# Optimization experiments

Hardware: AMD Instinct MI355X
Metric: run time of the kernel (lower is better)

## Reference

```python
import jax, jax.numpy as jnp
import numpy as np

B, F, L, P, H = 32, 64, 8192, 96, 8
HD = F // H
EPS_ATTN = 1e-6
EPS_REVIN = 1e-5
EPS_LN = 1e-5


def setup_inputs() -> dict:
    key = jax.random.key(0)
    ks = jax.random.split(key, 8)
    f32 = jnp.float32
    return {
        'x': jax.random.normal(ks[0], (B, F, L), dtype=f32),
        'gamma': jnp.ones((1, 1, F), dtype=f32),
        'beta': jnp.zeros((1, 1, F), dtype=f32),
        'ln_w': jnp.ones((F,), dtype=f32),
        'ln_b': jnp.zeros((F,), dtype=f32),
        'Wq': 0.05 * jax.random.normal(ks[1], (F, F), dtype=f32),
        'bq': jnp.zeros((F,), dtype=f32),
        'Wk': 0.05 * jax.random.normal(ks[2], (F, F), dtype=f32),
        'bk': jnp.zeros((F,), dtype=f32),
        'Wv': 0.05 * jax.random.normal(ks[3], (F, F), dtype=f32),
        'bv': jnp.zeros((F,), dtype=f32),
        'Wo': 0.05 * jax.random.normal(ks[4], (F, F), dtype=f32),
        'bo': jnp.zeros((F,), dtype=f32),
        'Wlin': 0.01 * jax.random.normal(ks[5], (P, L), dtype=f32),
        'blin': jnp.zeros((P,), dtype=f32),
        'Wp': 0.1 * jax.random.normal(ks[6], (1, F), dtype=f32),
        'bp': jnp.zeros((1,), dtype=f32),
    }


def _phi(t):
    # feature map: elu(x) + 1 (non-negative)
    return jax.nn.elu(t) + 1.0


def _layernorm(h, w, b):
    mu = jnp.mean(h, axis=-1, keepdims=True)
    var = jnp.mean(jnp.square(h - mu), axis=-1, keepdims=True)
    return (h - mu) * jax.lax.rsqrt(var + EPS_LN) * w + b


def reference(x, gamma, beta, ln_w, ln_b, Wq, bq, Wk, bk, Wv, bv, Wo, bo,
              Wlin, blin, Wp, bp):
    # (B, F, L) -> (B, L, F)
    xt = jnp.transpose(x, (0, 2, 1))
    # RevIN norm (stats over time axis, detached; torch std is unbiased ddof=1)
    mean = jax.lax.stop_gradient(jnp.mean(xt, axis=1, keepdims=True))
    std = jax.lax.stop_gradient(jnp.std(xt, axis=1, keepdims=True, ddof=1) + EPS_REVIN)
    xn = (xt - mean) / std * gamma + beta
    residual = xn
    h = _layernorm(xn, ln_w, ln_b)
    # Q/K/V projections (torch Linear: h @ W.T + b)
    Q = h @ Wq.T + bq
    K = h @ Wk.T + bk
    V = h @ Wv.T + bv
    # (B, L, F) -> (B, H, L, HD)
    def heads(t):
        return jnp.transpose(t.reshape(B, L, H, HD), (0, 2, 1, 3))
    Q, K, V = heads(Q), heads(K), heads(V)
    Q, K = _phi(Q), _phi(K)
    # linear attention: phi(Q) (phi(K)^T V) / (phi(Q) sum_n phi(K))
    KV = jnp.einsum('bhnd,bhne->bhde', K, V)           # (B,H,HD,HD)
    out = jnp.einsum('bhnd,bhde->bhne', Q, KV)          # (B,H,L,HD)
    Z = jnp.sum(K, axis=2)                              # (B,H,HD)
    normalizer = jnp.einsum('bhnd,bhd->bhn', Q, Z)[..., None] + EPS_ATTN
    out = out / normalizer
    out = jnp.transpose(out, (0, 2, 1, 3)).reshape(B, L, F)
    out = out @ Wo.T + bo
    y = out + residual                                  # (B, L, F)
    # temporal linear: (B, F, L) @ Wlin.T -> (B, F, P) -> (B, P, F)
    y = jnp.transpose(jnp.transpose(y, (0, 2, 1)) @ Wlin.T + blin, (0, 2, 1))
    # RevIN denorm
    y = (y - beta) / gamma
    y = y * std + mean
    # projector to scalar per step
    return (y @ Wp.T + bp)[..., 0]                      # (B, P)
```

## Files before the change

### kernel.cpp

```cpp
#include <hip/hip_runtime.h>
#include <cstddef>

#define NB 32
#define NF 64
#define NL 8192
#define NP 96
#define NH 8
#define TSPLIT 16

#define WS_MEAN 0
#define WS_STD  2048
#define WS_RSTD 4096
#define WS_KV   6144
#define WS_Z    22528
#define WS_OUT2 24576
#define WS_MUN  221184
#define WS_RSN  483328
#define WS_WLB  745472
#define WS_XNB  1138688
#define WS_YT   9527296
#define WS_WKV  17915904
#define WS_WQO  17920512
#define WS_SKT  17925120
#define WS_SQT  17925376

typedef __bf16 bfx8 __attribute__((ext_vector_type(8)));
typedef float f32x4 __attribute__((ext_vector_type(4)));
#define MFMA16(a, b, c) __builtin_amdgcn_mfma_f32_16x16x32_bf16((a), (b), (c), 0, 0, 0)

__device__ __forceinline__ unsigned short f2bf(float f) {
  unsigned u = __float_as_uint(f);
  unsigned r = u + 0x7FFFu + ((u >> 16) & 1u);
  return (unsigned short)(r >> 16);
}
__device__ __forceinline__ unsigned packbf2(float lo, float hi) {
  return (unsigned)f2bf(lo) | ((unsigned)f2bf(hi) << 16);
}
__device__ __forceinline__ float bflo(unsigned d) { return __uint_as_float(d << 16); }
__device__ __forceinline__ float bfhi(unsigned d) { return __uint_as_float(d & 0xFFFF0000u); }
__device__ __forceinline__ float bf1(unsigned short s) { return __uint_as_float(((unsigned)s) << 16); }

__device__ __forceinline__ bfx8 ldfrag(const unsigned short* p) {
  uint4 u = *(const uint4*)p;
  return __builtin_bit_cast(bfx8, u);
}

__global__ __launch_bounds__(256) void k_pre(
    const float* __restrict__ x, const float* __restrict__ Wlin,
    const float* __restrict__ lnw, const float* __restrict__ lnb,
    const float* __restrict__ Wk, const float* __restrict__ bk,
    const float* __restrict__ Wv, const float* __restrict__ bv,
    const float* __restrict__ Wq, const float* __restrict__ bq,
    const float* __restrict__ Wo,
    float* __restrict__ wmean, float* __restrict__ wstd, float* __restrict__ wrstd,
    unsigned short* __restrict__ wlb, float* __restrict__ zz,
    unsigned short* __restrict__ wWkv, unsigned short* __restrict__ wWqo,
    float* __restrict__ wSkT, float* __restrict__ wSqT) {
  __shared__ float r1[4], r2[4];
  const int bid = blockIdx.x, tid = threadIdx.x;
  if (bid < NB * NF) {
    const float4* row4 = (const float4*)(x + (size_t)bid * NL);
    float s1 = 0.f, s2 = 0.f;
#pragma unroll
    for (int i = 0; i < NL / 4 / 256; i++) {
      float4 v = row4[tid + i * 256];
      s1 += v.x + v.y + v.z + v.w;
      s2 += v.x * v.x + v.y * v.y + v.z * v.z + v.w * v.w;
    }
#pragma unroll
    for (int off = 32; off > 0; off >>= 1) {
      s1 += __shfl_down(s1, off, 64);
      s2 += __shfl_down(s2, off, 64);
    }
    if ((tid & 63) == 0) { r1[tid >> 6] = s1; r2[tid >> 6] = s2; }
    __syncthreads();
    if (tid == 0) {
      s1 = r1[0] + r1[1] + r1[2] + r1[3];
      s2 = r2[0] + r2[1] + r2[2] + r2[3];
      float m = s1 * (1.f / NL);
      float var = (s2 - (float)NL * m * m) * (1.f / (NL - 1));
      float sd = sqrtf(fmaxf(var, 0.f)) + 1e-5f;
      wmean[bid] = m;
      wstd[bid] = sd;
      wrstd[bid] = 1.f / sd;
    }
    unsigned zi = (unsigned)bid * 256u + (unsigned)tid;
    if (zi < 215040u) zz[zi] = 0.f;
  } else if (bid < NB * NF + NP * NL / 8 / 256) {
    int i = (bid - NB * NF) * 256 + tid;
    int p = i >> 10;
    int l8 = (i & 1023) * 8;
    float4 va = *(const float4*)&Wlin[(size_t)p * NL + l8];
    float4 vb = *(const float4*)&Wlin[(size_t)p * NL + l8 + 4];
    uint4 o;
    o.x = packbf2(va.x, va.y); o.y = packbf2(va.z, va.w);
    o.z = packbf2(vb.x, vb.y); o.w = packbf2(vb.z, vb.w);
    *(uint4*)&wlb[(((size_t)(l8 >> 5)) * NP + p) * 32 + (l8 & 31)] = o;
  } else if (bid == NB * NF + NP * NL / 8 / 256) {
    int jj = tid >> 2, g = tid & 3;
    int f0 = g * 16;
    float tkp = 0.f, tvp = 0.f, skp = 0.f, svp = 0.f;
#pragma unroll
    for (int i = 0; i < 4; i++) {
      int f = f0 + i * 4;
      float4 wk4 = *(const float4*)&Wk[jj * NF + f];
      float4 wv4 = *(const float4*)&Wv[jj * NF + f];
      float4 lw  = *(const float4*)&lnw[f];
      float4 lb  = *(const float4*)&lnb[f];
      uint2 pk2, pv2;
      pk2.x = packbf2(wk4.x * lw.x, wk4.y * lw.y);
      pk2.y = packbf2(wk4.z * lw.z, wk4.w * lw.w);
      pv2.x = packbf2(wv4.x * lw.x, wv4.y * lw.y);
      pv2.y = packbf2(wv4.z * lw.z, wv4.w * lw.w);
      *(uint2*)&wWkv[jj * 72 + f] = pk2;
      *(uint2*)&wWkv[4608 + jj * 72 + f] = pv2;
      tkp += lb.x * wk4.x + lb.y * wk4.y + lb.z * wk4.z + lb.w * wk4.w;
      tvp += lb.x * wv4.x + lb.y * wv4.y + lb.z * wv4.z + lb.w * wv4.w;
      skp += bflo(pk2.x) + bfhi(pk2.x) + bflo(pk2.y) + bfhi(pk2.y);
      svp += bflo(pv2.x) + bfhi(pv2.x) + bflo(pv2.y) + bfhi(pv2.y);
    }
    tkp += __shfl_xor(tkp, 1, 64); tkp += __shfl_xor(tkp, 2, 64);
    tvp += __shfl_xor(tvp, 1, 64); tvp += __shfl_xor(tvp, 2, 64);
    skp += __shfl_xor(skp, 1, 64); skp += __shfl_xor(skp, 2, 64);
    svp += __shfl_xor(svp, 1, 64); svp += __shfl_xor(svp, 2, 64);
    if (g == 0) {
      wSkT[jj]       = skp;
      wSkT[64 + jj]  = tkp + bk[jj];
      wSkT[128 + jj] = svp;
      wSkT[192 + jj] = tvp + bv[jj];
    }
  } else {
    int jj = tid >> 2, g = tid & 3;
    int f0 = g * 16;
    float tqp = 0.f, sqp = 0.f;
#pragma unroll
    for (int i = 0; i < 4; i++) {
      int f = f0 + i * 4;
      float4 wq4 = *(const float4*)&Wq[jj * NF + f];
      float4 wo4 = *(const float4*)&Wo[jj * NF + f];
      float4 lw  = *(const float4*)&lnw[f];
      float4 lb  = *(const float4*)&lnb[f];
      uint2 pq2, po2;
      pq2.x = packbf2(wq4.x * lw.x, wq4.y * lw.y);
      pq2.y = packbf2(wq4.z * lw.z, wq4.w * lw.w);
      po2.x = packbf2(wo4.x, wo4.y);
      po2.y = packbf2(wo4.z, wo4.w);
      *(uint2*)&wWqo[jj * 72 + f] = pq2;
      *(uint2*)&wWqo[4608 + jj * 72 + f] = po2;
      tqp += lb.x * wq4.x + lb.y * wq4.y + lb.z * wq4.z + lb.w * wq4.w;
      sqp += bflo(pq2.x) + bfhi(pq2.x) + bflo(pq2.y) + bfhi(pq2.y);
    }
    tqp += __shfl_xor(tqp, 1, 64); tqp += __shfl_xor(tqp, 2, 64);
    sqp += __shfl_xor(sqp, 1, 64); sqp += __shfl_xor(sqp, 2, 64);
    if (g == 0) { wSqT[jj] = sqp; wSqT[64 + jj] = tqp + bq[jj]; }
  }
}

__global__ __launch_bounds__(256, 4) void k_kv(
    const float* __restrict__ x,
    const float* __restrict__ gamma, const float* __restrict__ beta,
    const unsigned short* __restrict__ wWkv, const float* __restrict__ wSkT,
    const float* __restrict__ wmean, const float* __restrict__ wrstd,
    float* __restrict__ wKV, float* __restrict__ wZ,
    float* __restrict__ wmun, float* __restrict__ wrsn,
    unsigned short* __restrict__ xnb) {
  __shared__ __align__(16) char smem[20992];
  unsigned short* hA  = (unsigned short*)smem;
  unsigned short* pKh = (unsigned short*)smem;
  unsigned short* pVh = (unsigned short*)(smem + 9216);
  float* SkT = (float*)(smem + 18432);
  float* mun = (float*)(smem + 19456);
  float* rsn = (float*)(smem + 19968);
  float* cbc = (float*)(smem + 20480);

  const int tid = threadIdx.x;
  const int b = blockIdx.x >> 6;
  const int tI = blockIdx.x & 63;
  const int L0 = tI * 128;
  const int lane = tid & 63, wv = tid >> 6;
  const int mm = lane & 15, qd = lane >> 4;

  if (tid < 64) {
    float cb = wrstd[b * NF + tid] * gamma[tid];
    cbc[2 * tid] = cb;
    cbc[2 * tid + 1] = beta[tid] - wmean[b * NF + tid] * cb;
  }
  SkT[tid] = wSkT[tid];
  __syncthreads();

  {
    const int lt = tid >> 3;
    const int fg = tid & 7;
    const int l0q = lt * 4;
    const float* xp = x + ((size_t)(b * NF + fg * 8)) * NL + L0 + l0q;
    f32x4 v[8];
#pragma unroll
    for (int i = 0; i < 8; i++) v[i] = *(const f32x4*)(xp + (size_t)i * NL);
    float a[8][4];
#pragma unroll
    for (int i = 0; i < 4; i++) {
      float4 c = *(const float4*)&cbc[fg * 16 + i * 4];
#pragma unroll
      for (int j = 0; j < 4; j++) {
        a[2 * i][j]     = fmaf(v[2 * i][j], c.x, c.y);
        a[2 * i + 1][j] = fmaf(v[2 * i + 1][j], c.z, c.w);
      }
    }
    float s1[4], s2[4];
#pragma unroll
    for (int j = 0; j < 4; j++) {
      s1[j] = 0.f; s2[j] = 0.f;
#pragma unroll
      for (int i = 0; i < 8; i++) {
        s1[j] += a[i][j];
        s2[j] = fmaf(a[i][j], a[i][j], s2[j]);
      }
    }
#pragma unroll
    for (int m = 1; m <= 4; m <<= 1) {
#pragma unroll
      for (int j = 0; j < 4; j++) {
        s1[j] += __shfl_xor(s1[j], m, 64);
        s2[j] += __shfl_xor(s2[j], m, 64);
      }
    }
#pragma unroll
    for (int j = 0; j < 4; j++) {
      uint4 o;
      o.x = packbf2(a[0][j], a[1][j]);
      o.y = packbf2(a[2][j], a[3][j]);
      o.z = packbf2(a[4][j], a[5][j]);
      o.w = packbf2(a[6][j], a[7][j]);
      *(uint4*)&hA[(l0q + j) * 72 + fg * 8] = o;
      *(uint4*)(xnb + (((size_t)(b * 64 + tI) * 128 + l0q + j) * 64 + fg * 8)) = o;
    }
    if (fg == 0) {
      float mv[4], rv[4];
#pragma unroll
      for (int j = 0; j < 4; j++) {
        float mu = s1[j] * (1.f / NF);
        float var = s2[j] * (1.f / NF) - mu * mu;
        mv[j] = mu;
        rv[j] = rsqrtf(fmaxf(var, 0.f) + 1e-5f);
      }
      float4 m4 = {mv[0], mv[1], mv[2], mv[3]};
      float4 r4 = {rv[0], rv[1], rv[2], rv[3]};
      *(float4*)&mun[l0q] = m4;
      *(float4*)&rsn[l0q] = r4;
      *(float4*)&wmun[(size_t)b * NL + L0 + l0q] = m4;
      *(float4*)&wrsn[(size_t)b * NL + L0 + l0q] = r4;
    }
  }
  __syncthreads();

  const f32x4 fz = {0.f, 0.f, 0.f, 0.f};
  f32x4 kacc[2][4], vacc[2][4];
#pragma unroll
  for (int i = 0; i < 2; i++)
#pragma unroll
    for (int jt = 0; jt < 4; jt++) { kacc[i][jt] = fz; vacc[i][jt] = fz; }

#pragma unroll
  for (int kc = 0; kc < 2; kc++) {
    bfx8 a0 = ldfrag(&hA[(wv * 32 + mm) * 72 + kc * 32 + qd * 8]);
    bfx8 a1 = ldfrag(&hA[(wv * 32 + 16 + mm) * 72 + kc * 32 + qd * 8]);
#pragma unroll
    for (int jt = 0; jt < 4; jt++) {
      bfx8 bkf = ldfrag(&wWkv[(jt * 16 + mm) * 72 + kc * 32 + qd * 8]);
      bfx8 bvf = ldfrag(&wWkv[4608 + (jt * 16 + mm) * 72 + kc * 32 + qd * 8]);
      kacc[0][jt] = MFMA16(a0, bkf, kacc[0][jt]);
      kacc[1][jt] = MFMA16(a1, bkf, kacc[1][jt]);
      vacc[0][jt] = MFMA16(a0, bvf, vacc[0][jt]);
      vacc[1][jt] = MFMA16(a1, bvf, vacc[1][jt]);
    }
  }

#pragma unroll
  for (int lt2 = 0; lt2 < 2; lt2++) {
    float4 mu4 = *(const float4*)&mun[wv * 32 + lt2 * 16 + qd * 4];
    float4 rs4 = *(const float4*)&rsn[wv * 32 + lt2 * 16 + qd * 4];
    float muv[4] = {mu4.x, mu4.y, mu4.z, mu4.w};
    float rsv[4] = {rs4.x, rs4.y, rs4.z, rs4.w};
#pragma unroll
    for (int jt = 0; jt < 4; jt++) {
      int j = jt * 16 + mm;
      float Sk = SkT[j], Tk = SkT[64 + j], Sv = SkT[128 + j], Tv = SkT[192 + j];
#pragma unroll
      for (int r = 0; r < 4; r++) {
        float kk = rsv[r] * (kacc[lt2][jt][r] - muv[r] * Sk) + Tk;
        kacc[lt2][jt][r] = (kk > 0.f) ? (kk + 1.f) : __expf(kk);
        vacc[lt2][jt][r] = rsv[r] * (vacc[lt2][jt][r] - muv[r] * Sv) + Tv;
      }
    }
  }

  {
#pragma unroll
    for (int jt = 0; jt < 4; jt++) {
      float z = 0.f;
#pragma unroll
      for (int lt2 = 0; lt2 < 2; lt2++)
#pragma unroll
        for (int r = 0; r < 4; r++) z += kacc[lt2][jt][r];
      z += __shfl_xor(z, 16, 64);
      z += __shfl_xor(z, 32, 64);
      if (qd == 0) atomicAdd(&wZ[b * 64 + jt * 16 + mm], z);
    }
  }

  {
    f32x4 racc = fz;
#pragma unroll
    for (int h = 0; h < 2; h++) {
      __syncthreads();
      if ((wv >> 1) == h) {
#pragma unroll
        for (int lt2 = 0; lt2 < 2; lt2++) {
          int lcol = (wv & 1) * 32 + lt2 * 16 + qd * 4;
#pragma unroll
          for (int jt = 0; jt < 4; jt++) {
            int j = jt * 16 + mm;
            uint2 dk, dv;
            dk.x = packbf2(kacc[lt2][jt][0], kacc[lt2][jt][1]);
            dk.y = packbf2(kacc[lt2][jt][2], kacc[lt2][jt][3]);
            dv.x = packbf2(vacc[lt2][jt][0], vacc[lt2][jt][1]);
            dv.y = packbf2(vacc[lt2][jt][2], vacc[lt2][jt][3]);
            *(uint2*)&pKh[j * 72 + lcol] = dk;
            *(uint2*)&pVh[j * 72 + lcol] = dv;
          }
        }
      }
      __syncthreads();
#pragma unroll
      for (int kb = 0; kb < 2; kb++) {
        bfx8 ak  = ldfrag(&pKh[(wv * 16 + mm) * 72 + kb * 32 + qd * 8]);
        bfx8 bv8 = ldfrag(&pVh[(wv * 16 + mm) * 72 + kb * 32 + qd * 8]);
        racc = MFMA16(ak, bv8, racc);
      }
    }
    int eh = mm >> 3, e = mm & 7;
#pragma unroll
    for (int r = 0; r < 4; r++) {
      int row = qd * 4 + r;
      if ((row >> 3) == eh)
        atomicAdd(&wKV[(b * NH + wv * 2 + eh) * 64 + (row & 7) * 8 + e], racc[r]);
    }
  }
}

__global__ __launch_bounds__(256, 4) void k_qy(
    const unsigned short* __restrict__ xnb,
    const unsigned short* __restrict__ wWqo, const float* __restrict__ wSqT,
    const float* __restrict__ bo,
    const float* __restrict__ wmun, const float* __restrict__ wrsn,
    const float* __restrict__ wKV, const float* __restrict__ wZ,
    unsigned short* __restrict__ ytb) {
  __shared__ __align__(16) char smem[40960];
  unsigned short* hA  = (unsigned short*)smem;
  unsigned short* qaA = (unsigned short*)smem;
  unsigned short* WqB = (unsigned short*)(smem + 18432);
  unsigned short* WoB = (unsigned short*)(smem + 27648);
  float* kvz   = (float*)(smem + 36864);
  float* mun   = (float*)(smem + 39424);
  float* rsn   = (float*)(smem + 39936);
  float* SqTq  = (float*)(smem + 40448);

  const int tid = threadIdx.x;
  const int b = blockIdx.x >> 6;
  const int tI = blockIdx.x & 63;
  const int L0 = tI * 128;
  const int lane = tid & 63, wv = tid >> 6;
  const int mm = lane & 15, qd = lane >> 4;
  const unsigned short* xtile = xnb + (size_t)(b * 64 + tI) * 128 * 64;

  {
    uint4* dst = (uint4*)(smem + 18432);
    const uint4* src = (const uint4*)wWqo;
#pragma unroll
    for (int i = 0; i < 4; i++) dst[tid + i * 256] = src[tid + i * 256];
    if (tid < 128) dst[tid + 1024] = src[tid + 1024];
    if (tid < 128) SqTq[tid] = wSqT[tid];
  }
  for (int i = tid; i < 640; i += 256)
    kvz[i] = (i < 512) ? wKV[b * 512 + i] : (i < 576 ? wZ[b * 64 + i - 512] : bo[i - 576]);
  {
    int row = tid >> 1, half = tid & 1;
    const uint4* s4 = (const uint4*)(xtile + (size_t)row * 64 + half * 32);
    uint4 u0 = s4[0], u1 = s4[1], u2 = s4[2], u3 = s4[3];
    uint4* d4 = (uint4*)&hA[row * 72 + half * 32];
    d4[0] = u0; d4[1] = u1; d4[2] = u2; d4[3] = u3;
  }
  if (tid < 64) {
    int h = tid >> 5, i = tid & 31;
    const float* src = h ? wrsn : wmun;
    float4 v = *(const float4*)&src[(size_t)b * NL + L0 + i * 4];
    *(float4*)&((h ? rsn : mun)[i * 4]) = v;
  }
  __syncthreads();

  const f32x4 fz = {0.f, 0.f, 0.f, 0.f};

  {
    f32x4 qacc[2][4];
#pragma unroll
    for (int i = 0; i < 2; i++)
#pragma unroll
      for (int jt = 0; jt < 4; jt++) qacc[i][jt] = fz;
#pragma unroll
    for (int kc = 0; kc < 2; kc++) {
      bfx8 a0 = ldfrag(&hA[(wv * 32 + mm) * 72 + kc * 32 + qd * 8]);
      bfx8 a1 = ldfrag(&hA[(wv * 32 + 16 + mm) * 72 + kc * 32 + qd * 8]);
#pragma unroll
      for (int jt = 0; jt < 4; jt++) {
        bfx8 bqf = ldfrag(&WqB[(jt * 16 + mm) * 72 + kc * 32 + qd * 8]);
        qacc[0][jt] = MFMA16(a0, bqf, qacc[0][jt]);
        qacc[1][jt] = MFMA16(a1, bqf, qacc[1][jt]);
      }
    }
#pragma unroll
    for (int lt2 = 0; lt2 < 2; lt2++) {
      float4 mu4 = *(const float4*)&mun[wv * 32 + lt2 * 16 + qd * 4];
      float4 rs4 = *(const float4*)&rsn[wv * 32 + lt2 * 16 + qd * 4];
      float muv[4] = {mu4.x, mu4.y, mu4.z, mu4.w};
      float rsv[4] = {rs4.x, rs4.y, rs4.z, rs4.w};
      int l0 = wv * 32 + lt2 * 16 + qd * 4;
#pragma unroll
      for (int jt = 0; jt < 4; jt++) {
        int j = jt * 16 + mm;
        float Sj = SqTq[j], Tj = SqTq[64 + j];
#pragma unroll
        for (int r = 0; r < 4; r++) {
          float q = rsv[r] * (qacc[lt2][jt][r] - muv[r] * Sj) + Tj;
          q = (q > 0.f) ? (q + 1.f) : __expf(q);
          qaA[(l0 + r) * 72 + j] = f2bf(q);
        }
      }
    }
  }
  __syncthreads();

  {
    int lt = tid & 31, hd = tid >> 5;
#pragma unroll
    for (int hp = 0; hp < 2; hp++) {
      int lbase = lt * 4 + hp * 2;
      float qv[2][8];
#pragma unroll
      for (int i = 0; i < 2; i++) {
        uint4 u = *(const uint4*)&qaA[(lbase + i) * 72 + hd * 8];
        qv[i][0] = bflo(u.x); qv[i][1] = bfhi(u.x);
        qv[i][2] = bflo(u.y); qv[i][3] = bfhi(u.y);
        qv[i][4] = bflo(u.z); qv[i][5] = bfhi(u.z);
        qv[i][6] = bflo(u.w); qv[i][7] = bfhi(u.w);
      }
      float att[2][8], nrm[2];
#pragma unroll
      for (int i = 0; i < 2; i++) {
        nrm[i] = 1e-6f;
#pragma unroll
        for (int e = 0; e < 8; e++) att[i][e] = 0.f;
      }
#pragma unroll
      for (int d = 0; d < 8; d++) {
        float zd = kvz[512 + hd * 8 + d];
        float4 kva = *(const float4*)&kvz[hd * 64 + d * 8];
        float4 kvb = *(const float4*)&kvz[hd * 64 + d * 8 + 4];
#pragma unroll
        for (int i = 0; i < 2; i++) {
          float qq = qv[i][d];
          nrm[i] = fmaf(qq, zd, nrm[i]);
          att[i][0] = fmaf(qq, kva.x, att[i][0]);
          att[i][1] = fmaf(qq, kva.y, att[i][1]);
          att[i][2] = fmaf(qq, kva.z, att[i][2]);
          att[i][3] = fmaf(qq, kva.w, att[i][3]);
          att[i][4] = fmaf(qq, kvb.x, att[i][4]);
          att[i][5] = fmaf(qq, kvb.y, att[i][5]);
          att[i][6] = fmaf(qq, kvb.z, att[i][6]);
          att[i][7] = fmaf(qq, kvb.w, att[i][7]);
        }
      }
#pragma unroll
      for (int i = 0; i < 2; i++) {
        float inv = 1.f / nrm[i];
        uint4 o;
        o.x = packbf2(att[i][0] * inv, att[i][1] * inv);
        o.y = packbf2(att[i][2] * inv, att[i][3] * inv);
        o.z = packbf2(att[i][4] * inv, att[i][5] * inv);
        o.w = packbf2(att[i][6] * inv, att[i][7] * inv);
        *(uint4*)&qaA[(lbase + i) * 72 + hd * 8] = o;
      }
    }
  }
  __syncthreads();

  {
    f32x4 yacc[2][4];
#pragma unroll
    for (int i = 0; i < 2; i++)
#pragma unroll
      for (int ft = 0; ft < 4; ft++) yacc[i][ft] = fz;
#pragma unroll
    for (int ec = 0; ec < 2; ec++) {
      bfx8 a0 = ldfrag(&qaA[(wv * 32 + mm) * 72 + ec * 32 + qd * 8]);
      bfx8 a1 = ldfrag(&qaA[(wv * 32 + 16 + mm) * 72 + ec * 32 + qd * 8]);
#pragma unroll
      for (int ft = 0; ft < 4; ft++) {
        bfx8 bof = ldfrag(&WoB[(ft * 16 + mm) * 72 + ec * 32 + qd * 8]);
        yacc[0][ft] = MFMA16(a0, bof, yacc[0][ft]);
        yacc[1][ft] = MFMA16(a1, bof, yacc[1][ft]);
      }
    }
#pragma unroll
    for (int lt2 = 0; lt2 < 2; lt2++) {
      int l0 = wv * 32 + lt2 * 16 + qd * 4;
#pragma unroll
      for (int ft = 0; ft < 4; ft++) {
        int ff = ft * 16 + mm;
        float bof = kvz[576 + ff];
        float v0 = yacc[lt2][ft][0] + bf1(xtile[(size_t)(l0 + 0) * 64 + ff]) + bof;
        float v1 = yacc[lt2][ft][1] + bf1(xtile[(size_t)(l0 + 1) * 64 + ff]) + bof;
        float v2 = yacc[lt2][ft][2] + bf1(xtile[(size_t)(l0 + 2) * 64 + ff]) + bof;
        float v3 = yacc[lt2][ft][3] + bf1(xtile[(size_t)(l0 + 3) * 64 + ff]) + bof;
        uint2 o2;
        o2.x = packbf2(v0, v1);
        o2.y = packbf2(v2, v3);
        size_t idx = (((size_t)b * (NL / 32) + (L0 >> 5) + wv) * 64 + ff) * 32 + lt2 * 16 + qd * 4;
        *(uint2*)&ytb[idx] = o2;
      }
    }
  }
}

__global__ __launch_bounds__(256) void k_temporal(
    const unsigned short* __restrict__ ytb, const unsigned short* __restrict__ wlb,
    float* __restrict__ out2) {
  const int tid = threadIdx.x, lane = tid & 63, wvx = tid >> 6;
  const int mm = lane & 15, qd = lane >> 4;
  const int b = blockIdx.x / TSPLIT;
  const int kc = blockIdx.x % TSPLIT;
  const f32x4 fz = {0.f, 0.f, 0.f, 0.f};
  f32x4 acc[6];
#pragma unroll
  for (int pt = 0; pt < 6; pt++) acc[pt] = fz;

#pragma unroll 2
  for (int ks = 0; ks < NL / 32 / TSPLIT; ks++) {
    int lg = kc * (NL / 32 / TSPLIT) + ks;
    bfx8 bfr = ldfrag(&ytb[(((size_t)b * (NL / 32) + lg) * 64 + wvx * 16 + mm) * 32 + qd * 8]);
#pragma unroll
    for (int pt = 0; pt < 6; pt++) {
      bfx8 afr = ldfrag(&wlb[((size_t)lg * NP + pt * 16 + mm) * 32 + qd * 8]);
      acc[pt] = MFMA16(afr, bfr, acc[pt]);
    }
  }
  const int ff = wvx * 16 + mm;
#pragma unroll
  for (int pt = 0; pt < 6; pt++) {
#pragma unroll
    for (int r = 0; r < 4; r++) {
      int p = pt * 16 + qd * 4 + r;
      atomicAdd(&out2[((size_t)(b * NP + p)) * NF + ff], acc[pt][r]);
    }
  }
}

__global__ __launch_bounds__(256) void k_final(
    const float* __restrict__ out2, const float* __restrict__ blin,
    const float* __restrict__ gamma, const float* __restrict__ beta,
    const float* __restrict__ wmean, const float* __restrict__ wstd,
    const float* __restrict__ Wp, const float* __restrict__ bp0,
    float* __restrict__ out) {
  int bp = blockIdx.x * 4 + (threadIdx.x >> 6);
  int f = threadIdx.x & 63;
  int b = bp / NP, p = bp % NP;
  float v = out2[(size_t)bp * NF + f] + blin[p];
  v = (v - beta[f]) / gamma[f];
  v = v * wstd[b * NF + f] + wmean[b * NF + f];
  float s = v * Wp[f];
#pragma unroll
  for (int off = 32; off > 0; off >>= 1)
    s += __shfl_down(s, off, 64);
  if (f == 0) out[bp] = s + bp0[0];
}

extern "C" void kernel_launch(void* const* d_in, const int* in_sizes, int n_in,
                              void* d_out, int out_size, void* d_ws, size_t ws_size,
                              hipStream_t stream) {
  const float* x     = (const float*)d_in[0];
  const float* gamma = (const float*)d_in[1];
  const float* beta  = (const float*)d_in[2];
  const float* lnw   = (const float*)d_in[3];
  const float* lnb   = (const float*)d_in[4];
  const float* Wq    = (const float*)d_in[5];
  const float* bq    = (const float*)d_in[6];
  const float* Wk    = (const float*)d_in[7];
  const float* bk    = (const float*)d_in[8];
  const float* Wv    = (const float*)d_in[9];
  const float* bv    = (const float*)d_in[10];
  const float* Wo    = (const float*)d_in[11];
  const float* bo    = (const float*)d_in[12];
  const float* Wlin  = (const float*)d_in[13];
  const float* blin  = (const float*)d_in[14];
  const float* Wp    = (const float*)d_in[15];
  const float* bp    = (const float*)d_in[16];
  float* out = (float*)d_out;
  float* ws  = (float*)d_ws;

  float* wmean = ws + WS_MEAN;
  float* wstd  = ws + WS_STD;
  float* wrstd = ws + WS_RSTD;
  float* wKV   = ws + WS_KV;
  float* wZ    = ws + WS_Z;
  float* wout2 = ws + WS_OUT2;
  float* wmun  = ws + WS_MUN;
  float* wrsn  = ws + WS_RSN;
  unsigned short* wlb = (unsigned short*)(ws + WS_WLB);
  unsigned short* xnb = (unsigned short*)(ws + WS_XNB);
  unsigned short* ytb = (unsigned short*)(ws + WS_YT);
  unsigned short* wWkv = (unsigned short*)(ws + WS_WKV);
  unsigned short* wWqo = (unsigned short*)(ws + WS_WQO);
  float* wSkT = ws + WS_SKT;
  float* wSqT = ws + WS_SQT;

  k_pre<<<NB * NF + NP * NL / 8 / 256 + 2, 256, 0, stream>>>(
      x, Wlin, lnw, lnb, Wk, bk, Wv, bv, Wq, bq, Wo,
      wmean, wstd, wrstd, wlb, wKV, wWkv, wWqo, wSkT, wSqT);
  k_kv<<<NB * 64, 256, 0, stream>>>(x, gamma, beta, wWkv, wSkT,
                                    wmean, wrstd, wKV, wZ, wmun, wrsn, xnb);
  k_qy<<<NB * 64, 256, 0, stream>>>(xnb, wWqo, wSqT, bo,
                                    wmun, wrsn, wKV, wZ, ytb);
  k_temporal<<<NB * TSPLIT, 256, 0, stream>>>(ytb, wlb, wout2);
  k_final<<<NB * NP / 4, 256, 0, stream>>>(wout2, blin, gamma, beta, wmean, wstd, Wp, bp, out);
}
```

Before: 210.6 us.

## Fuse temporal linear into k_qy via LDS-staged y tile and atomics

Removes the k_temporal kernel and the bf16 y intermediate in global memory. Each k_qy block now stages its 128-step output tile in shared memory and multiplies it by the matching Wlin slice with MFMA. It then atomically adds the partial (P,F) results into one of two out2 copies chosen by tile parity, and k_final sums the two copies. This saves a global round trip of about 33MB plus a kernel launch, but adds many more atomics (64 tiles per batch instead of 16 splits), extra Wlin reads per block, and a larger zeroed workspace.

```diff
diff --git a/kernel.cpp b/kernel.cpp
--- a/kernel.cpp
+++ b/kernel.cpp
@@ -6,7 +6,6 @@
 #define NL 8192
 #define NP 96
 #define NH 8
-#define TSPLIT 16
 
 #define WS_MEAN 0
 #define WS_STD  2048
@@ -14,15 +13,14 @@
 #define WS_KV   6144
 #define WS_Z    22528
 #define WS_OUT2 24576
-#define WS_MUN  221184
-#define WS_RSN  483328
-#define WS_WLB  745472
-#define WS_XNB  1138688
-#define WS_YT   9527296
-#define WS_WKV  17915904
-#define WS_WQO  17920512
-#define WS_SKT  17925120
-#define WS_SQT  17925376
+#define WS_MUN  417792
+#define WS_RSN  679936
+#define WS_WLB  942080
+#define WS_XNB  1335296
+#define WS_WKV  9723904
+#define WS_WQO  9728512
+#define WS_SKT  9733120
+#define WS_SQT  9733376
 
 typedef __bf16 bfx8 __attribute__((ext_vector_type(8)));
 typedef float f32x4 __attribute__((ext_vector_type(4)));
@@ -85,7 +83,7 @@
       wrstd[bid] = 1.f / sd;
     }
     unsigned zi = (unsigned)bid * 256u + (unsigned)tid;
-    if (zi < 215040u) zz[zi] = 0.f;
+    if (zi < 411648u) zz[zi] = 0.f;
   } else if (bid < NB * NF + NP * NL / 8 / 256) {
     int i = (bid - NB * NF) * 256 + tid;
     int p = i >> 10;
@@ -354,7 +352,7 @@
     const float* __restrict__ bo,
     const float* __restrict__ wmun, const float* __restrict__ wrsn,
     const float* __restrict__ wKV, const float* __restrict__ wZ,
-    unsigned short* __restrict__ ytb) {
+    const unsigned short* __restrict__ wlb, float* __restrict__ out2) {
   __shared__ __align__(16) char smem[40960];
   unsigned short* hA  = (unsigned short*)smem;
   unsigned short* qaA = (unsigned short*)smem;
@@ -510,6 +508,8 @@
         yacc[1][ft] = MFMA16(a1, bof, yacc[1][ft]);
       }
     }
+    __syncthreads();
+    unsigned short* yl = (unsigned short*)smem;
 #pragma unroll
     for (int lt2 = 0; lt2 < 2; lt2++) {
       int l0 = wv * 32 + lt2 * 16 + qd * 4;
@@ -524,42 +524,36 @@
         uint2 o2;
         o2.x = packbf2(v0, v1);
         o2.y = packbf2(v2, v3);
-        size_t idx = (((size_t)b * (NL / 32) + (L0 >> 5) + wv) * 64 + ff) * 32 + lt2 * 16 + qd * 4;
-        *(uint2*)&ytb[idx] = o2;
-      }
-    }
-  }
-}
-
-__global__ __launch_bounds__(256) void k_temporal(
-    const unsigned short* __restrict__ ytb, const unsigned short* __restrict__ wlb,
-    float* __restrict__ out2) {
-  const int tid = threadIdx.x, lane = tid & 63, wvx = tid >> 6;
-  const int mm = lane & 15, qd = lane >> 4;
-  const int b = blockIdx.x / TSPLIT;
-  const int kc = blockIdx.x % TSPLIT;
-  const f32x4 fz = {0.f, 0.f, 0.f, 0.f};
-  f32x4 acc[6];
-#pragma unroll
-  for (int pt = 0; pt < 6; pt++) acc[pt] = fz;
-
-#pragma unroll 2
-  for (int ks = 0; ks < NL / 32 / TSPLIT; ks++) {
-    int lg = kc * (NL / 32 / TSPLIT) + ks;
-    bfx8 bfr = ldfrag(&ytb[(((size_t)b * (NL / 32) + lg) * 64 + wvx * 16 + mm) * 32 + qd * 8]);
+        *(uint2*)&yl[ff * 140 + l0] = o2;
+      }
+    }
+  }
+  __syncthreads();
+
+  {
+    const unsigned short* yl = (const unsigned short*)smem;
+    const unsigned short* wlbL = wlb + (size_t)(L0 >> 5) * NP * 32;
+    f32x4 acc[6];
+#pragma unroll
+    for (int pt = 0; pt < 6; pt++) acc[pt] = fz;
+#pragma unroll
+    for (int lg2 = 0; lg2 < 4; lg2++) {
+      bfx8 bfr = ldfrag(&yl[(wv * 16 + mm) * 140 + lg2 * 32 + qd * 8]);
+#pragma unroll
+      for (int pt = 0; pt < 6; pt++) {
+        bfx8 afr = ldfrag(&wlbL[((size_t)lg2 * NP + pt * 16 + mm) * 32 + qd * 8]);
+        acc[pt] = MFMA16(afr, bfr, acc[pt]);
+      }
+    }
+    float* o2s = out2 + (size_t)(tI & 1) * (NB * NP * NF);
+    const int ff2 = wv * 16 + mm;
 #pragma unroll
     for (int pt = 0; pt < 6; pt++) {
-      bfx8 afr = ldfrag(&wlb[((size_t)lg * NP + pt * 16 + mm) * 32 + qd * 8]);
-      acc[pt] = MFMA16(afr, bfr, acc[pt]);
-    }
-  }
-  const int ff = wvx * 16 + mm;
-#pragma unroll
-  for (int pt = 0; pt < 6; pt++) {
-#pragma unroll
-    for (int r = 0; r < 4; r++) {
-      int p = pt * 16 + qd * 4 + r;
-      atomicAdd(&out2[((size_t)(b * NP + p)) * NF + ff], acc[pt][r]);
+#pragma unroll
+      for (int r = 0; r < 4; r++) {
+        int p = pt * 16 + qd * 4 + r;
+        atomicAdd(&o2s[((size_t)(b * NP + p)) * NF + ff2], acc[pt][r]);
+      }
     }
   }
 }
@@ -573,7 +567,8 @@
   int bp = blockIdx.x * 4 + (threadIdx.x >> 6);
   int f = threadIdx.x & 63;
   int b = bp / NP, p = bp % NP;
-  float v = out2[(size_t)bp * NF + f] + blin[p];
+  float v = out2[(size_t)bp * NF + f] + out2[(size_t)(NB * NP * NF) + (size_t)bp * NF + f]
+          + blin[p];
   v = (v - beta[f]) / gamma[f];
   v = v * wstd[b * NF + f] + wmean[b * NF + f];
   float s = v * Wp[f];
@@ -616,7 +611,6 @@
   float* wrsn  = ws + WS_RSN;
   unsigned short* wlb = (unsigned short*)(ws + WS_WLB);
   unsigned short* xnb = (unsigned short*)(ws + WS_XNB);
-  unsigned short* ytb = (unsigned short*)(ws + WS_YT);
   unsigned short* wWkv = (unsigned short*)(ws + WS_WKV);
   unsigned short* wWqo = (unsigned short*)(ws + WS_WQO);
   float* wSkT = ws + WS_SKT;
@@ -628,7 +622,6 @@
   k_kv<<<NB * 64, 256, 0, stream>>>(x, gamma, beta, wWkv, wSkT,
                                     wmean, wrstd, wKV, wZ, wmun, wrsn, xnb);
   k_qy<<<NB * 64, 256, 0, stream>>>(xnb, wWqo, wSqT, bo,
-                                    wmun, wrsn, wKV, wZ, ytb);
-  k_temporal<<<NB * TSPLIT, 256, 0, stream>>>(ytb, wlb, wout2);
+                                    wmun, wrsn, wKV, wZ, wlb, wout2);
   k_final<<<NB * NP / 4, 256, 0, stream>>>(wout2, blin, gamma, beta, wmean, wstd, Wp, bp, out);
 }
```

Result: no change. 213.1 us (+1.2%).
